# Kernel optimization log

Measured on AMD Instinct MI355X. Metric: run time of the kernel, lower is better.

The kernel has to match this reference:

```python
import jax, jax.numpy as jnp
import numpy as np
import math

B, N, Q, K = 1, 64, 512, 512
C_Q = C_K = C_V = 256
C_HIDDEN = 32
NO_HEADS = 8
HID = C_HIDDEN * NO_HEADS  # 256


def setup_inputs() -> dict:
    key = jax.random.key(0)
    ks = jax.random.split(key, 12)
    inp = {
        "q_x": jax.random.normal(ks[0], (B, N, Q, C_Q), jnp.float32),
        "k_x": jax.random.normal(ks[1], (B, N, K, C_K), jnp.float32),
        "v_x": jax.random.normal(ks[2], (B, N, K, C_V), jnp.float32),
        "bias_mask": jax.random.normal(ks[3], (B, N, 1, 1, K), jnp.float32),
        "bias_pair": jax.random.normal(ks[4], (B, 1, NO_HEADS, Q, K), jnp.float32),
        # projection weights stored [in, out] (torch Linear is [out, in])
        "wq": jax.random.normal(ks[5], (C_Q, HID), jnp.float32) / math.sqrt(C_Q),
        "wk": jax.random.normal(ks[6], (C_K, HID), jnp.float32) / math.sqrt(C_K),
        "wv": jax.random.normal(ks[7], (C_V, HID), jnp.float32) / math.sqrt(C_V),
        # gating: init weights=0, bias=1 in the module; use small random for a non-trivial test
        "wg": jax.random.normal(ks[8], (C_Q, HID), jnp.float32) * 0.02,
        "bg": jnp.ones((HID,), jnp.float32),
        # output: init 'final' (zeros); use small random for a non-trivial test
        "wo": jax.random.normal(ks[9], (HID, C_Q), jnp.float32) * 0.02,
        "bo": jnp.zeros((C_Q,), jnp.float32),
    }
    return inp


def reference(q_x, k_x, v_x, bias_mask, bias_pair, wq, wk, wv, wg, bg, wo, bo):
    h, c = NO_HEADS, C_HIDDEN
    # projections -> [B, N, Q/K, H, C_h]
    q = (q_x @ wq).reshape(*q_x.shape[:-1], h, c) / math.sqrt(c)
    k = (k_x @ wk).reshape(*k_x.shape[:-1], h, c)
    v = (v_x @ wv).reshape(*v_x.shape[:-1], h, c)
    # logits [B, N, H, Q, K] with additive biases
    a = jnp.einsum("bnqhc,bnkhc->bnhqk", q, k) + bias_mask + bias_pair
    a = jax.nn.softmax(a, axis=-1)
    # output [B, N, Q, H, C_h]
    o = jnp.einsum("bnhqk,bnkhc->bnqhc", a, v)
    # gating
    g = jax.nn.sigmoid((q_x @ wg + bg).reshape(*q_x.shape[:-1], h, c))
    o = o * g
    o = o.reshape(*o.shape[:-2], h * c)
    return o @ wo + bo
```

## Files before the change

kernel.cpp:

```cpp
#include <hip/hip_runtime.h>
#include <math.h>

#define NSEQ   64
#define QLEN   512
#define KLEN   512
#define CIN    256
#define HEADS  8
#define CH     32
#define HIDDIM 256
#define M_TOTAL (NSEQ * QLEN)

typedef _Float16 f16x8 __attribute__((ext_vector_type(8)));
typedef _Float16 f16x4 __attribute__((ext_vector_type(4)));
typedef __fp16   fp16x2 __attribute__((ext_vector_type(2)));
typedef float    f32x4 __attribute__((ext_vector_type(4)));

__device__ __forceinline__ void gload16(const void* g, void* l) {
    __builtin_amdgcn_global_load_lds(
        (const __attribute__((address_space(1))) void*)g,
        (__attribute__((address_space(3))) void*)l, 16, 0, 0);
}

__global__ __launch_bounds__(256) void wcast_kernel(
    const float* __restrict__ w0, const float* __restrict__ w1,
    const float* __restrict__ w2, const float* __restrict__ w3,
    const float* __restrict__ w4, _Float16* __restrict__ wt)
{
    __shared__ float t[64][65];
    const float* W;
    switch (blockIdx.z) {
        case 0: W = w0; break; case 1: W = w1; break;
        case 2: W = w2; break; case 3: W = w3; break;
        default: W = w4;
    }
    _Float16* WT = wt + (size_t)blockIdx.z * 65536;
    const int i0 = blockIdx.x * 64, o0 = blockIdx.y * 64;
    const int tid = threadIdx.x;
    const int rr = tid >> 4, c4 = tid & 15;
    #pragma unroll
    for (int i = 0; i < 4; ++i) {
        const int row = rr + i * 16;
        *(float4*)&t[row][c4 * 4] = *(const float4*)&W[(size_t)(i0 + row) * 256 + o0 + c4 * 4];
    }
    __syncthreads();
    #pragma unroll
    for (int i = 0; i < 4; ++i) {
        const int row = rr + i * 16;
        f16x4 v;
        #pragma unroll
        for (int j = 0; j < 4; ++j) v[j] = (_Float16)t[c4 * 4 + j][row];
        *(f16x4*)&WT[(size_t)(o0 + row) * 256 + i0 + c4 * 4] = v;
    }
}

__global__ __launch_bounds__(256) void bpfrag_kernel(
    const float* __restrict__ bias_pair, float* __restrict__ frag)
{
    __shared__ float t[64][68];
    const int qb = blockIdx.x, kb = blockIdx.y, h = blockIdx.z;
    const int tid = threadIdx.x;
    #pragma unroll
    for (int i = 0; i < 4; ++i) {
        const int idx = tid + i * 256;
        const int r = idx >> 4, c4 = idx & 15;
        *(float4*)&t[r][c4 * 4] = *(const float4*)
            &bias_pair[((size_t)h * QLEN + qb * 64 + r) * KLEN + kb * 64 + c4 * 4];
    }
    __syncthreads();
    const int lane = tid & 63, w = tid >> 6;
    const int l15 = lane & 15, quad = lane >> 4;
    const int qt = qb * 4 + w;
    #pragma unroll
    for (int kt2 = 0; kt2 < 4; ++kt2) {
        const int kt = kb * 4 + kt2;
        float4 v;
        v.x = t[w * 16 + l15][kt2 * 16 + quad * 4 + 0];
        v.y = t[w * 16 + l15][kt2 * 16 + quad * 4 + 1];
        v.z = t[w * 16 + l15][kt2 * 16 + quad * 4 + 2];
        v.w = t[w * 16 + l15][kt2 * 16 + quad * 4 + 3];
        *(float4*)&frag[(((size_t)(h * 32 + qt) * 32) + kt) * 256 + lane * 4] = v;
    }
}

__global__ __launch_bounds__(256, 2) void proj_gemm_kernel(
    const float* __restrict__ q_x, const float* __restrict__ k_x,
    const float* __restrict__ v_x, const _Float16* __restrict__ wT,
    const float* __restrict__ bg,
    _Float16* __restrict__ oq, _Float16* __restrict__ ok,
    _Float16* __restrict__ ovT, _Float16* __restrict__ og)
{
    __shared__ _Float16 A_s[128][72];
    __shared__ __attribute__((aligned(16))) _Float16 B_s[2][128 * 64];

    const int mode = (blockIdx.z << 1) | (blockIdx.y >> 1);
    const float* A = (mode <= 1) ? q_x : (mode == 2) ? k_x : v_x;
    const _Float16* BT = wT + (size_t)mode * 65536;
    const int m0 = blockIdx.x * 128;
    const int n0 = (blockIdx.y & 1) * 128;
    const int tid = threadIdx.x;
    const int lane = tid & 63, w = tid >> 6;
    const int l15 = lane & 15, quad = lane >> 4;
    const int mw = (w & 1) * 64, nw = (w >> 1) * 64;
    const int ar = tid >> 3, aseg = tid & 7;

    f32x4 acc[4][4];
    #pragma unroll
    for (int mt = 0; mt < 4; ++mt)
        #pragma unroll
        for (int nt = 0; nt < 4; ++nt) acc[mt][nt] = (f32x4){0.f, 0.f, 0.f, 0.f};

    float4 alo[4], ahi[4];
    #pragma unroll
    for (int it = 0; it < 4; ++it) {
        const float* ap = A + (size_t)(m0 + ar + it * 32) * CIN + aseg * 8;
        alo[it] = *(const float4*)ap;
        ahi[it] = *(const float4*)(ap + 4);
    }
    #pragma unroll
    for (int j = 0; j < 4; ++j) {
        const int p = tid + j * 256;
        const int r = p >> 3;
        const int lc = (p & 7) ^ (r & 7);
        gload16(BT + (size_t)(n0 + r) * CIN + lc * 8, &B_s[0][p * 8]);
    }
    #pragma unroll
    for (int it = 0; it < 4; ++it) {
        f16x8 v;
        v[0] = (_Float16)alo[it].x; v[1] = (_Float16)alo[it].y;
        v[2] = (_Float16)alo[it].z; v[3] = (_Float16)alo[it].w;
        v[4] = (_Float16)ahi[it].x; v[5] = (_Float16)ahi[it].y;
        v[6] = (_Float16)ahi[it].z; v[7] = (_Float16)ahi[it].w;
        *(f16x8*)&A_s[ar + it * 32][aseg * 8] = v;
    }
    __syncthreads();

    int buf = 0;
    for (int kk = 0; kk < 4; ++kk) {
        if (kk < 3) {
            const int k0n = (kk + 1) * 64;
            #pragma unroll
            for (int it = 0; it < 4; ++it) {
                const float* ap = A + (size_t)(m0 + ar + it * 32) * CIN + k0n + aseg * 8;
                alo[it] = *(const float4*)ap;
                ahi[it] = *(const float4*)(ap + 4);
            }
            #pragma unroll
            for (int j = 0; j < 4; ++j) {
                const int p = tid + j * 256;
                const int r = p >> 3;
                const int lc = (p & 7) ^ (r & 7);
                gload16(BT + (size_t)(n0 + r) * CIN + k0n + lc * 8, &B_s[buf ^ 1][p * 8]);
            }
        }
        #pragma unroll
        for (int ks = 0; ks < 2; ++ks) {
            f16x8 af[4], bf[4];
            #pragma unroll
            for (int mt = 0; mt < 4; ++mt)
                af[mt] = *(const f16x8*)&A_s[mw + mt * 16 + l15][ks * 32 + quad * 8];
            #pragma unroll
            for (int nt = 0; nt < 4; ++nt) {
                const int brow = nw + nt * 16 + l15;
                const int bc = (ks * 4 + quad) ^ (brow & 7);
                bf[nt] = *(const f16x8*)&B_s[buf][brow * 64 + bc * 8];
            }
            #pragma unroll
            for (int mt = 0; mt < 4; ++mt)
                #pragma unroll
                for (int nt = 0; nt < 4; ++nt)
                    acc[mt][nt] = __builtin_amdgcn_mfma_f32_16x16x32_f16(
                        af[mt], bf[nt], acc[mt][nt], 0, 0, 0);
        }
        if (kk < 3) {
            __syncthreads();
            #pragma unroll
            for (int it = 0; it < 4; ++it) {
                f16x8 v;
                v[0] = (_Float16)alo[it].x; v[1] = (_Float16)alo[it].y;
                v[2] = (_Float16)alo[it].z; v[3] = (_Float16)alo[it].w;
                v[4] = (_Float16)ahi[it].x; v[5] = (_Float16)ahi[it].y;
                v[6] = (_Float16)ahi[it].z; v[7] = (_Float16)ahi[it].w;
                *(f16x8*)&A_s[ar + it * 32][aseg * 8] = v;
            }
            __syncthreads();
            buf ^= 1;
        }
    }

    #pragma unroll
    for (int mt = 0; mt < 4; ++mt) {
        #pragma unroll
        for (int nt = 0; nt < 4; ++nt) {
            const int col = n0 + nw + nt * 16 + l15;
            const int rowb = m0 + mw + mt * 16 + quad * 4;
            if (mode == 3) {
                const int nn = rowb >> 9, kpos = rowb & 511;
                f16x4 st;
                #pragma unroll
                for (int reg = 0; reg < 4; ++reg) st[reg] = (_Float16)acc[mt][nt][reg];
                *(f16x4*)&ovT[((size_t)(nn * 256 + col)) * 512 + kpos] = st;
            } else {
                _Float16* C = (mode == 0) ? oq : (mode == 1) ? og : ok;
                #pragma unroll
                for (int reg = 0; reg < 4; ++reg) {
                    float x = acc[mt][nt][reg];
                    if (mode == 0) x *= 0.17677669529663689f;
                    if (mode == 1) { x += bg[col]; x = 1.0f / (1.0f + __expf(-x)); }
                    C[(size_t)(rowb + reg) * HIDDIM + col] = (_Float16)x;
                }
            }
        }
    }
}

__global__ __launch_bounds__(256, 2) void gemm_mfma_kernel(
    const _Float16* __restrict__ Ain, const _Float16* __restrict__ BT,
    const float* __restrict__ bias, float* __restrict__ Cout)
{
    __shared__ __attribute__((aligned(16))) _Float16 A_s[2][128 * 64];
    __shared__ __attribute__((aligned(16))) _Float16 B_s[2][128 * 64];
    const int m0 = blockIdx.x * 128, n0 = blockIdx.y * 128;
    const int tid = threadIdx.x;
    const int lane = tid & 63, w = tid >> 6;
    const int l15 = lane & 15, quad = lane >> 4;
    const int mw = (w & 1) * 64, nw = (w >> 1) * 64;

    f32x4 acc[4][4];
    #pragma unroll
    for (int mt = 0; mt < 4; ++mt)
        #pragma unroll
        for (int nt = 0; nt < 4; ++nt) acc[mt][nt] = (f32x4){0.f, 0.f, 0.f, 0.f};

    #pragma unroll
    for (int j = 0; j < 4; ++j) {
        const int p = tid + j * 256;
        const int r = p >> 3;
        const int lc = (p & 7) ^ (r & 7);
        gload16(Ain + (size_t)(m0 + r) * CIN + lc * 8, &A_s[0][p * 8]);
        gload16(BT  + (size_t)(n0 + r) * CIN + lc * 8, &B_s[0][p * 8]);
    }
    __syncthreads();

    int buf = 0;
    for (int kk = 0; kk < 4; ++kk) {
        if (kk < 3) {
            const int k0n = (kk + 1) * 64;
            #pragma unroll
            for (int j = 0; j < 4; ++j) {
                const int p = tid + j * 256;
                const int r = p >> 3;
                const int lc = (p & 7) ^ (r & 7);
                gload16(Ain + (size_t)(m0 + r) * CIN + k0n + lc * 8, &A_s[buf ^ 1][p * 8]);
                gload16(BT  + (size_t)(n0 + r) * CIN + k0n + lc * 8, &B_s[buf ^ 1][p * 8]);
            }
        }
        #pragma unroll
        for (int ks = 0; ks < 2; ++ks) {
            f16x8 af[4], bf[4];
            #pragma unroll
            for (int mt = 0; mt < 4; ++mt) {
                const int arow = mw + mt * 16 + l15;
                const int ac = (ks * 4 + quad) ^ (arow & 7);
                af[mt] = *(const f16x8*)&A_s[buf][arow * 64 + ac * 8];
            }
            #pragma unroll
            for (int nt = 0; nt < 4; ++nt) {
                const int brow = nw + nt * 16 + l15;
                const int bc = (ks * 4 + quad) ^ (brow & 7);
                bf[nt] = *(const f16x8*)&B_s[buf][brow * 64 + bc * 8];
            }
            #pragma unroll
            for (int mt = 0; mt < 4; ++mt)
                #pragma unroll
                for (int nt = 0; nt < 4; ++nt)
                    acc[mt][nt] = __builtin_amdgcn_mfma_f32_16x16x32_f16(
                        af[mt], bf[nt], acc[mt][nt], 0, 0, 0);
        }
        if (kk < 3) { __syncthreads(); buf ^= 1; }
    }

    #pragma unroll
    for (int mt = 0; mt < 4; ++mt) {
        #pragma unroll
        for (int nt = 0; nt < 4; ++nt) {
            const int col = n0 + nw + nt * 16 + l15;
            const int rowb = m0 + mw + mt * 16 + quad * 4;
            #pragma unroll
            for (int reg = 0; reg < 4; ++reg) {
                const float x = acc[mt][nt][reg] + bias[col];
                Cout[(size_t)(rowb + reg) * HIDDIM + col] = x;
            }
        }
    }
}

__global__ __launch_bounds__(256, 4) void attn_kernel(
    const _Float16* __restrict__ qb, const _Float16* __restrict__ kb,
    const _Float16* __restrict__ vT, const _Float16* __restrict__ gb,
    _Float16* __restrict__ ob,
    const float* __restrict__ bias_mask, const float* __restrict__ bp_frag)
{
    __shared__ _Float16 k_s[128][40];
    __shared__ _Float16 v_s[32][136];

    const int n    = blockIdx.x;
    const int h    = blockIdx.y;
    const int q0   = blockIdx.z * 128;
    const int tid  = threadIdx.x;
    const int lane = tid & 63;
    const int wq   = tid >> 6;
    const int l15  = lane & 15;
    const int quad = lane >> 4;

    f16x8 qf[2];
    #pragma unroll
    for (int qt = 0; qt < 2; ++qt)
        qf[qt] = *(const f16x8*)(qb +
            (size_t)(n * QLEN + q0 + wq * 32 + qt * 16 + l15) * HIDDIM + h * CH + quad * 8);

    const float* bpf = bp_frag +
        ((size_t)(h * 32 + blockIdx.z * 8 + wq * 2) * 32) * 256 + lane * 4;
    const float* bmb = bias_mask + n * KLEN + quad * 4;

    f32x4 o_acc[2][2];
    float l_lane[2] = {0.f, 0.f};
    #pragma unroll
    for (int qt = 0; qt < 2; ++qt)
        #pragma unroll
        for (int ct = 0; ct < 2; ++ct) o_acc[qt][ct] = (f32x4){0.f, 0.f, 0.f, 0.f};

    const f32x4 z4 = (f32x4){0.f, 0.f, 0.f, 0.f};

    for (int ch = 0; ch < 4; ++ch) {
        __syncthreads();
        #pragma unroll
        for (int i = 0; i < 2; ++i) {
            const int idx = tid + i * 256;
            const int r = idx >> 2, c8 = idx & 3;
            *(uint4*)&k_s[r][c8 * 8] = *(const uint4*)
                (kb + (size_t)(n * KLEN + ch * 128 + r) * HIDDIM + h * CH + c8 * 8);
            const int vr = idx >> 4, vs = idx & 15;
            *(uint4*)&v_s[vr][vs * 8] = *(const uint4*)
                (vT + ((size_t)(n * HEADS + h) * CH + vr) * KLEN + ch * 128 + vs * 8);
        }
        __syncthreads();

        #pragma unroll
        for (int kt = 0; kt < 8; ++kt) {
            const int kti = ch * 8 + kt;
            const f16x8 kf = *(const f16x8*)&k_s[kt * 16 + l15][quad * 8];
            const f32x4 s0 = __builtin_amdgcn_mfma_f32_16x16x32_f16(kf, qf[0], z4, 0, 0, 0);
            const f32x4 s1 = __builtin_amdgcn_mfma_f32_16x16x32_f16(kf, qf[1], z4, 0, 0, 0);
            const float4 bm = *(const float4*)(bmb + ch * 128 + kt * 16);
            const f16x4 bv0 = *(const f16x4*)&v_s[l15][kt * 16 + quad * 4];
            const f16x4 bv1 = *(const f16x4*)&v_s[16 + l15][kt * 16 + quad * 4];
            #pragma unroll
            for (int qt = 0; qt < 2; ++qt) {
                const f32x4 s = qt ? s1 : s0;
                const float4 bp = *(const float4*)(bpf + ((size_t)qt * 32 + kti) * 256);
                const float p0 = __expf(s[0] + bm.x + bp.x - 4.0f);
                const float p1 = __expf(s[1] + bm.y + bp.y - 4.0f);
                const float p2 = __expf(s[2] + bm.z + bp.z - 4.0f);
                const float p3 = __expf(s[3] + bm.w + bp.w - 4.0f);
                l_lane[qt] += (p0 + p1) + (p2 + p3);
                union { f16x4 v; fp16x2 h[2]; } u;
                u.h[0] = __builtin_amdgcn_cvt_pkrtz(p0, p1);
                u.h[1] = __builtin_amdgcn_cvt_pkrtz(p2, p3);
                o_acc[qt][0] = __builtin_amdgcn_mfma_f32_16x16x16f16(u.v, bv0, o_acc[qt][0], 0, 0, 0);
                o_acc[qt][1] = __builtin_amdgcn_mfma_f32_16x16x16f16(u.v, bv1, o_acc[qt][1], 0, 0, 0);
            }
        }
    }

    float invl[2][4];
    #pragma unroll
    for (int qt = 0; qt < 2; ++qt) {
        float lf = l_lane[qt];
        lf += __shfl_xor(lf, 16);
        lf += __shfl_xor(lf, 32);
        #pragma unroll
        for (int reg = 0; reg < 4; ++reg)
            invl[qt][reg] = 1.0f / __shfl(lf, quad * 4 + reg);
    }

    #pragma unroll
    for (int qt = 0; qt < 2; ++qt) {
        #pragma unroll
        for (int ct = 0; ct < 2; ++ct) {
            #pragma unroll
            for (int reg = 0; reg < 4; ++reg) {
                const int row = q0 + wq * 32 + qt * 16 + quad * 4 + reg;
                const size_t idx = (size_t)(n * QLEN + row) * HIDDIM + h * CH + ct * 16 + l15;
                const float g = (float)gb[idx];
                ob[idx] = (_Float16)(o_acc[qt][ct][reg] * invl[qt][reg] * g);
            }
        }
    }
}

extern "C" void kernel_launch(void* const* d_in, const int* in_sizes, int n_in,
                              void* d_out, int out_size, void* d_ws, size_t ws_size,
                              hipStream_t stream)
{
    const float* q_x       = (const float*)d_in[0];
    const float* k_x       = (const float*)d_in[1];
    const float* v_x       = (const float*)d_in[2];
    const float* bias_mask = (const float*)d_in[3];
    const float* bias_pair = (const float*)d_in[4];
    const float* wq        = (const float*)d_in[5];
    const float* wk        = (const float*)d_in[6];
    const float* wv        = (const float*)d_in[7];
    const float* wg        = (const float*)d_in[8];
    const float* bg        = (const float*)d_in[9];
    const float* wo        = (const float*)d_in[10];
    const float* bo        = (const float*)d_in[11];
    float* out = (float*)d_out;

    const size_t BUF = (size_t)M_TOTAL * HIDDIM;
    _Float16* ws_q  = (_Float16*)d_ws;
    _Float16* ws_k  = ws_q + BUF;
    _Float16* ws_vT = ws_k + BUF;
    _Float16* ws_g  = ws_vT + BUF;
    _Float16* ws_o  = ws_g + BUF;
    _Float16* wT    = ws_o + BUF;
    float*    bpf   = (float*)(wT + 5 * 65536);

    wcast_kernel<<<dim3(4, 4, 5), 256, 0, stream>>>(wq, wg, wk, wv, wo, wT);
    bpfrag_kernel<<<dim3(8, 8, 8), 256, 0, stream>>>(bias_pair, bpf);

    proj_gemm_kernel<<<dim3(M_TOTAL / 128, 4, 2), 256, 0, stream>>>(
        q_x, k_x, v_x, wT, bg, ws_q, ws_k, ws_vT, ws_g);

    attn_kernel<<<dim3(NSEQ, HEADS, QLEN / 128), 256, 0, stream>>>(
        ws_q, ws_k, ws_vT, ws_g, ws_o, bias_mask, bpf);

    gemm_mfma_kernel<<<dim3(M_TOTAL / 128, 2), 256, 0, stream>>>(
        ws_o, wT + 4 * 65536, bo, out);
}
```

Before: 272.5 us.

## Restructure projection GEMM into persistent blocks with register-resident weights

The projection GEMM now runs as 512 persistent blocks. Each block keeps a 128-column slice of the fp16 weight matrix in registers for all of K=256, then streams 16 panels of 32 fp32 rows through double-buffered, swizzled LDS using async global-to-LDS loads. Each panel is converted to fp16 on read and written out before the next. This removes the repeated weight tile loads and the register round-trip for the A conversion. In exchange there are fewer blocks and heavy register use, the per-panel epilogue and barrier are serialized, and the blocks read the A activations twice, once for each N half.

```diff
diff --git a/kernel.cpp b/kernel.cpp
--- a/kernel.cpp
+++ b/kernel.cpp
@@ -89,127 +89,121 @@
     _Float16* __restrict__ oq, _Float16* __restrict__ ok,
     _Float16* __restrict__ ovT, _Float16* __restrict__ og)
 {
-    __shared__ _Float16 A_s[128][72];
-    __shared__ __attribute__((aligned(16))) _Float16 B_s[2][128 * 64];
-
-    const int mode = (blockIdx.z << 1) | (blockIdx.y >> 1);
+    __shared__ __attribute__((aligned(16))) float A_s[2][32 * 256];
+
+    const int combo = blockIdx.x >> 6;
+    const int blk   = blockIdx.x & 63;
+    const int mode  = combo >> 1;
+    const int nhalf = combo & 1;
     const float* A = (mode <= 1) ? q_x : (mode == 2) ? k_x : v_x;
     const _Float16* BT = wT + (size_t)mode * 65536;
-    const int m0 = blockIdx.x * 128;
-    const int n0 = (blockIdx.y & 1) * 128;
-    const int tid = threadIdx.x;
+
+    const int tid  = threadIdx.x;
     const int lane = tid & 63, w = tid >> 6;
-    const int l15 = lane & 15, quad = lane >> 4;
-    const int mw = (w & 1) * 64, nw = (w >> 1) * 64;
-    const int ar = tid >> 3, aseg = tid & 7;
-
-    f32x4 acc[4][4];
-    #pragma unroll
-    for (int mt = 0; mt < 4; ++mt)
-        #pragma unroll
-        for (int nt = 0; nt < 4; ++nt) acc[mt][nt] = (f32x4){0.f, 0.f, 0.f, 0.f};
-
-    float4 alo[4], ahi[4];
-    #pragma unroll
-    for (int it = 0; it < 4; ++it) {
-        const float* ap = A + (size_t)(m0 + ar + it * 32) * CIN + aseg * 8;
-        alo[it] = *(const float4*)ap;
-        ahi[it] = *(const float4*)(ap + 4);
-    }
-    #pragma unroll
-    for (int j = 0; j < 4; ++j) {
-        const int p = tid + j * 256;
-        const int r = p >> 3;
-        const int lc = (p & 7) ^ (r & 7);
-        gload16(BT + (size_t)(n0 + r) * CIN + lc * 8, &B_s[0][p * 8]);
-    }
-    #pragma unroll
-    for (int it = 0; it < 4; ++it) {
-        f16x8 v;
-        v[0] = (_Float16)alo[it].x; v[1] = (_Float16)alo[it].y;
-        v[2] = (_Float16)alo[it].z; v[3] = (_Float16)alo[it].w;
-        v[4] = (_Float16)ahi[it].x; v[5] = (_Float16)ahi[it].y;
-        v[6] = (_Float16)ahi[it].z; v[7] = (_Float16)ahi[it].w;
-        *(f16x8*)&A_s[ar + it * 32][aseg * 8] = v;
-    }
+    const int l15  = lane & 15, quad = lane >> 4;
+    const int nw   = nhalf * 128 + w * 32;
+
+    f16x8 bfr[2][8];
+    #pragma unroll
+    for (int nt = 0; nt < 2; ++nt)
+        #pragma unroll
+        for (int ks = 0; ks < 8; ++ks)
+            bfr[nt][ks] = *(const f16x8*)(BT +
+                (size_t)(nw + nt * 16 + l15) * 256 + ks * 32 + quad * 8);
+
+    float bgv[2] = {0.f, 0.f};
+    if (mode == 1) { bgv[0] = bg[nw + l15]; bgv[1] = bg[nw + 16 + l15]; }
+
+    const int row_base = blk * 512;
+
+    f32x4 acc[2][2];
+    #pragma unroll
+    for (int mt = 0; mt < 2; ++mt)
+        #pragma unroll
+        for (int nt = 0; nt < 2; ++nt) acc[mt][nt] = (f32x4){0.f, 0.f, 0.f, 0.f};
+
+    auto stage = [&](int panel, int buf) {
+        const int row0 = row_base + panel * 32;
+        #pragma unroll
+        for (int j = 0; j < 8; ++j) {
+            const int p = tid + j * 256;
+            const int r = p >> 6, c = p & 63;
+            const int cl = (c & ~7) | ((c & 7) ^ (r & 7));
+            gload16(A + (size_t)(row0 + r) * 256 + cl * 4, &A_s[buf][p * 4]);
+        }
+    };
+
+    stage(0, 0);
     __syncthreads();
 
-    int buf = 0;
-    for (int kk = 0; kk < 4; ++kk) {
-        if (kk < 3) {
-            const int k0n = (kk + 1) * 64;
-            #pragma unroll
-            for (int it = 0; it < 4; ++it) {
-                const float* ap = A + (size_t)(m0 + ar + it * 32) * CIN + k0n + aseg * 8;
-                alo[it] = *(const float4*)ap;
-                ahi[it] = *(const float4*)(ap + 4);
-            }
-            #pragma unroll
-            for (int j = 0; j < 4; ++j) {
-                const int p = tid + j * 256;
-                const int r = p >> 3;
-                const int lc = (p & 7) ^ (r & 7);
-                gload16(BT + (size_t)(n0 + r) * CIN + k0n + lc * 8, &B_s[buf ^ 1][p * 8]);
-            }
-        }
-        #pragma unroll
-        for (int ks = 0; ks < 2; ++ks) {
-            f16x8 af[4], bf[4];
-            #pragma unroll
-            for (int mt = 0; mt < 4; ++mt)
-                af[mt] = *(const f16x8*)&A_s[mw + mt * 16 + l15][ks * 32 + quad * 8];
-            #pragma unroll
-            for (int nt = 0; nt < 4; ++nt) {
-                const int brow = nw + nt * 16 + l15;
-                const int bc = (ks * 4 + quad) ^ (brow & 7);
-                bf[nt] = *(const f16x8*)&B_s[buf][brow * 64 + bc * 8];
-            }
-            #pragma unroll
-            for (int mt = 0; mt < 4; ++mt)
+    for (int i = 0; i < 16; ++i) {
+        if (i < 15) stage(i + 1, (i + 1) & 1);
+        const int buf = i & 1;
+
+        #pragma unroll
+        for (int ks = 0; ks < 8; ++ks) {
+            f16x8 af[2];
+            #pragma unroll
+            for (int mt = 0; mt < 2; ++mt) {
+                const int r  = mt * 16 + l15;
+                const int x0 = ks * 8 + ((quad * 2 + 0) ^ (r & 7));
+                const int x1 = ks * 8 + ((quad * 2 + 1) ^ (r & 7));
+                const f32x4 a0 = *(const f32x4*)&A_s[buf][(r * 64 + x0) * 4];
+                const f32x4 a1 = *(const f32x4*)&A_s[buf][(r * 64 + x1) * 4];
+                f16x8 v;
+                v[0] = (_Float16)a0[0]; v[1] = (_Float16)a0[1];
+                v[2] = (_Float16)a0[2]; v[3] = (_Float16)a0[3];
+                v[4] = (_Float16)a1[0]; v[5] = (_Float16)a1[1];
+                v[6] = (_Float16)a1[2]; v[7] = (_Float16)a1[3];
+                af[mt] = v;
+            }
+            #pragma unroll
+            for (int mt = 0; mt < 2; ++mt)
                 #pragma unroll
-                for (int nt = 0; nt < 4; ++nt)
+                for (int nt = 0; nt < 2; ++nt)
                     acc[mt][nt] = __builtin_amdgcn_mfma_f32_16x16x32_f16(
-                        af[mt], bf[nt], acc[mt][nt], 0, 0, 0);
-        }
-        if (kk < 3) {
-            __syncthreads();
-            #pragma unroll
-            for (int it = 0; it < 4; ++it) {
-                f16x8 v;
-                v[0] = (_Float16)alo[it].x; v[1] = (_Float16)alo[it].y;
-                v[2] = (_Float16)alo[it].z; v[3] = (_Float16)alo[it].w;
-                v[4] = (_Float16)ahi[it].x; v[5] = (_Float16)ahi[it].y;
-                v[6] = (_Float16)ahi[it].z; v[7] = (_Float16)ahi[it].w;
-                *(f16x8*)&A_s[ar + it * 32][aseg * 8] = v;
-            }
-            __syncthreads();
-            buf ^= 1;
-        }
-    }
-
-    #pragma unroll
-    for (int mt = 0; mt < 4; ++mt) {
-        #pragma unroll
-        for (int nt = 0; nt < 4; ++nt) {
-            const int col = n0 + nw + nt * 16 + l15;
-            const int rowb = m0 + mw + mt * 16 + quad * 4;
-            if (mode == 3) {
-                const int nn = rowb >> 9, kpos = rowb & 511;
-                f16x4 st;
+                        af[mt], bfr[nt][ks], acc[mt][nt], 0, 0, 0);
+        }
+
+        const int row0 = row_base + i * 32;
+        if (mode == 3) {
+            #pragma unroll
+            for (int mt = 0; mt < 2; ++mt) {
                 #pragma unroll
-                for (int reg = 0; reg < 4; ++reg) st[reg] = (_Float16)acc[mt][nt][reg];
-                *(f16x4*)&ovT[((size_t)(nn * 256 + col)) * 512 + kpos] = st;
-            } else {
-                _Float16* C = (mode == 0) ? oq : (mode == 1) ? og : ok;
+                for (int nt = 0; nt < 2; ++nt) {
+                    const int col  = nw + nt * 16 + l15;
+                    const int rowg = row0 + mt * 16 + quad * 4;
+                    const int nn = rowg >> 9, kpos = rowg & 511;
+                    f16x4 st;
+                    #pragma unroll
+                    for (int reg = 0; reg < 4; ++reg) st[reg] = (_Float16)acc[mt][nt][reg];
+                    *(f16x4*)&ovT[((size_t)(nn * 256 + col)) * 512 + kpos] = st;
+                }
+            }
+        } else {
+            _Float16* C = (mode == 0) ? oq : (mode == 1) ? og : ok;
+            #pragma unroll
+            for (int mt = 0; mt < 2; ++mt) {
                 #pragma unroll
-                for (int reg = 0; reg < 4; ++reg) {
-                    float x = acc[mt][nt][reg];
-                    if (mode == 0) x *= 0.17677669529663689f;
-                    if (mode == 1) { x += bg[col]; x = 1.0f / (1.0f + __expf(-x)); }
-                    C[(size_t)(rowb + reg) * HIDDIM + col] = (_Float16)x;
+                for (int nt = 0; nt < 2; ++nt) {
+                    const int col  = nw + nt * 16 + l15;
+                    const int rowg = row0 + mt * 16 + quad * 4;
+                    #pragma unroll
+                    for (int reg = 0; reg < 4; ++reg) {
+                        float x = acc[mt][nt][reg];
+                        if (mode == 0) x *= 0.17677669529663689f;
+                        if (mode == 1) { x += bgv[nt]; x = 1.0f / (1.0f + __expf(-x)); }
+                        C[(size_t)(rowg + reg) * HIDDIM + col] = (_Float16)x;
+                    }
                 }
             }
         }
+        #pragma unroll
+        for (int mt = 0; mt < 2; ++mt)
+            #pragma unroll
+            for (int nt = 0; nt < 2; ++nt) acc[mt][nt] = (f32x4){0.f, 0.f, 0.f, 0.f};
+
+        __syncthreads();
     }
 }
 
@@ -428,7 +422,7 @@
     wcast_kernel<<<dim3(4, 4, 5), 256, 0, stream>>>(wq, wg, wk, wv, wo, wT);
     bpfrag_kernel<<<dim3(8, 8, 8), 256, 0, stream>>>(bias_pair, bpf);
 
-    proj_gemm_kernel<<<dim3(M_TOTAL / 128, 4, 2), 256, 0, stream>>>(
+    proj_gemm_kernel<<<dim3(512), 256, 0, stream>>>(
         q_x, k_x, v_x, wT, bg, ws_q, ws_k, ws_vT, ws_g);
 
     attn_kernel<<<dim3(NSEQ, HEADS, QLEN / 128), 256, 0, stream>>>(
```

New measurement: 263.7 us. 1.03x faster.
